# Kernel optimization log

Measured on AMD Instinct MI355X. Metric: run time of the kernel, lower is better.

The kernel has to match this reference:

```python
import jax, jax.numpy as jnp
import numpy as np

EPS = 1e-7   # keras.backend.epsilon() added before log in ctc_batch_cost
NEG = -1e30  # log-space 'zero'

B, T, C, L = 256, 1024, 96, 64


def setup_inputs() -> dict:
    key = jax.random.key(0)
    k1, k2 = jax.random.split(key)
    y_true = jax.random.randint(k1, (B, L), 0, C - 1, dtype=jnp.int32)  # labels in [0, C-2], blank = C-1
    y_pred = jax.random.uniform(k2, (B, T, C), dtype=jnp.float32)
    y_pred = y_pred / jnp.sum(y_pred, axis=-1, keepdims=True)  # valid softmax-like probabilities
    return {"y_true": y_true, "y_pred": y_pred}


def _ctc_loss(y_pred, y_true):
    # Faithful re-implementation of keras.backend.ctc_batch_cost with
    # input_length = T and label_length = L for every batch row.
    b, t, c = y_pred.shape
    l = y_true.shape[1]
    blank = c - 1
    s = 2 * l + 1  # extended label length (blanks interleaved)

    logp = jnp.log(y_pred + EPS)  # [B, T, C]

    # extended label sequence: blank, l0, blank, l1, ..., blank
    ext = jnp.full((b, s), blank, dtype=y_true.dtype).at[:, 1::2].set(y_true)  # [B, S]

    # emission log-probs per (t, b, s)
    lp = jnp.take_along_axis(logp, jnp.broadcast_to(ext[:, None, :], (b, t, s)), axis=2)  # [B, T, S]
    lp = jnp.transpose(lp, (1, 0, 2))  # [T, B, S]

    # skip transition s-2 -> s allowed iff ext[s] != blank and ext[s] != ext[s-2]
    ext_m2 = jnp.pad(ext, ((0, 0), (2, 0)), constant_values=-1)[:, :s]
    skip_ok = (ext != blank) & (ext != ext_m2)  # [B, S]

    alpha0 = jnp.full((b, s), NEG, dtype=logp.dtype)
    alpha0 = alpha0.at[:, 0].set(lp[0, :, 0]).at[:, 1].set(lp[0, :, 1])

    def step(alpha, lp_t):
        a1 = jnp.pad(alpha, ((0, 0), (1, 0)), constant_values=NEG)[:, :s]
        a2 = jnp.pad(alpha, ((0, 0), (2, 0)), constant_values=NEG)[:, :s]
        a2 = jnp.where(skip_ok, a2, NEG)
        new = jax.nn.logsumexp(jnp.stack([alpha, a1, a2]), axis=0) + lp_t
        return new, None

    alpha, _ = jax.lax.scan(step, alpha0, lp[1:])

    loss = -jax.nn.logsumexp(jnp.stack([alpha[:, s - 1], alpha[:, s - 2]]), axis=0)
    return loss[:, None]  # [B, 1], matching ctc_batch_cost


def reference(y_true, y_pred):
    return _ctc_loss(y_pred, y_true)
```

## Files before the change

kernel.cpp:

```cpp
#include <hip/hip_runtime.h>
#include <cstdint>


constexpr int BB = 256;
constexpr int TT = 1024;
constexpr int CC = 96;
constexpr int LL = 64;
constexpr int CT = 64;
constexpr int NCH = TT / CT;
constexpr int CHUNK_FLOATS = CT * CC;
constexpr int CHUNK_BYTES  = CHUNK_FLOATS*4;
#define EPSF 1e-7f

__device__ __forceinline__ float wf_shr1_f(float v) {
  int r = __builtin_amdgcn_update_dpp(0, __float_as_int(v), 0x138 , 0xF, 0xF, false);
  return __int_as_float(r);
}

template <int CTRL>
__device__ __forceinline__ float dpp_max(float v) {
  int r = __builtin_amdgcn_update_dpp(__float_as_int(v), __float_as_int(v), CTRL, 0xF, 0xF, false);
  return fmaxf(v, __int_as_float(r));
}

__device__ __forceinline__ void async16(void* lds, const void* g) {
  __builtin_amdgcn_global_load_lds((const __attribute__((address_space(1))) void*)g,
                                   (__attribute__((address_space(3))) void*)lds,
                                   16, 0, 0);
}

__global__ void __launch_bounds__(64, 1)
ctc_fwd(const int* __restrict__ y_true, const float* __restrict__ y_pred,
        float* __restrict__ out) {
  __shared__ alignas(16) float buf[2][CHUNK_FLOATS];
  const int b    = blockIdx.x;
  const int lane = threadIdx.x;

  const int lab  = y_true[b * LL + lane];
  const int labp = __builtin_amdgcn_update_dpp(-1, lab, 0x138, 0xF, 0xF, false);
  const float mskip = (lane > 0 && lab != labp) ? 1.0f : 0.0f;

  const char* src = (const char*)(y_pred + (size_t)b * (TT * CC));

  {
    const char* g0 = src + lane * 16;
#pragma unroll
    for (int j = 0; j < 24; ++j) async16((char*)&buf[0][0] + j * 1024, g0 + j * 1024);
    const char* g1 = src + CHUNK_BYTES + lane * 16;
#pragma unroll
    for (int j = 0; j < 24; ++j) async16((char*)&buf[1][0] + j * 1024, g1 + j * 1024);
  }

  float a0 = (lane == 0) ? 1.0f : 0.0f;
  float a1 = 0.0f;
  float a2 = 0.0f;
  int   scale = 0;

  for (int c = 0; c < NCH; ++c) {
    if (c < NCH - 1) asm volatile("s_waitcnt vmcnt(24)" ::: "memory");
    else             asm volatile("s_waitcnt vmcnt(0)"  ::: "memory");

    const float* bp = &buf[c & 1][0];
#pragma unroll
    for (int g8 = 0; g8 < 8; ++g8) {
#pragma unroll
      for (int u = 0; u < 8; ++u) {
        const int r = g8 * 8 + u;
        const float pl  = bp[r * CC + lab] + EPSF;
        const float pb  = bp[r * CC + (CC - 1)] + EPSF;
        const float a1p = wf_shr1_f(a1);
        const float na0 = (a0 + a1p) * pb;
        float s3 = a1 + a0;
        s3 = fmaf(a1p, mskip, s3);
        const float na1 = s3 * pl;
        const float na2 = (a2 + a1) * pb;
        a0 = na0; a1 = na1; a2 = na2;
      }
      float m = fmaxf(fmaxf(a0, a1), a2);
      m = dpp_max<0x111>(m);
      m = dpp_max<0x112>(m);
      m = dpp_max<0x114>(m);
      m = dpp_max<0x118>(m);
      m = dpp_max<0x142>(m);
      m = dpp_max<0x143>(m);
      const int mb = __builtin_amdgcn_readlane(__float_as_int(m), 63);
      const int k  = 227 - ((mb >> 23) & 0xFF);
      scale += k;
      a0 = ldexpf(a0, k);
      a1 = ldexpf(a1, k);
      a2 = ldexpf(a2, k);
    }

    if (c + 2 < NCH) {
      const char* g = src + (size_t)(c + 2) * CHUNK_BYTES + lane * 16;
      char* l = (char*)&buf[c & 1][0];
#pragma unroll
      for (int j = 0; j < 24; ++j) async16(l + j * 1024, g + j * 1024);
    }
  }

  if (lane == 63) {
    const float s = a1 + a2;
    out[b] = 0.693147180559945f * ((float)scale - log2f(s));
  }
}

extern "C" void kernel_launch(void* const* d_in, const int* in_sizes, int n_in,
                              void* d_out, int out_size, void* d_ws, size_t ws_size,
                              hipStream_t stream) {
  (void)in_sizes; (void)n_in; (void)d_ws; (void)ws_size; (void)out_size;
  const int*   y_true = (const int*)d_in[0];
  const float* y_pred = (const float*)d_in[1];
  float*       out    = (float*)d_out;
  ctc_fwd<<<BB, 64, 0, stream>>>(y_true, y_pred, out);
}
```

Before: 160.6 us.

## Replace LDS chunk staging with register-prefetched direct gathers of needed columns

Drops the 24KB-per-chunk async global-to-LDS copies of the full class dimension. Each lane now loads only the two probabilities it needs (its label and the blank) straight from global memory into a 4-slot register ring, prefetching 8-timestep groups three groups ahead. Rescaling now runs every 16 steps instead of every 8, with the exponent target lowered to leave headroom. This cuts the bytes moved and removes LDS traffic, at the cost of scattered 4-byte global loads whose latency must be hidden by the register pipeline.

```diff
diff --git a/kernel.cpp b/kernel.cpp
--- a/kernel.cpp
+++ b/kernel.cpp
@@ -6,10 +6,9 @@
 constexpr int TT = 1024;
 constexpr int CC = 96;
 constexpr int LL = 64;
-constexpr int CT = 64;
-constexpr int NCH = TT / CT;
-constexpr int CHUNK_FLOATS = CT * CC;
-constexpr int CHUNK_BYTES  = CHUNK_FLOATS*4;
+constexpr int G  = 8;
+constexpr int NG = TT / G;
+constexpr int SL = 4;
 #define EPSF 1e-7f
 
 __device__ __forceinline__ float wf_shr1_f(float v) {
@@ -23,16 +22,9 @@
   return fmaxf(v, __int_as_float(r));
 }
 
-__device__ __forceinline__ void async16(void* lds, const void* g) {
-  __builtin_amdgcn_global_load_lds((const __attribute__((address_space(1))) void*)g,
-                                   (__attribute__((address_space(3))) void*)lds,
-                                   16, 0, 0);
-}
-
 __global__ void __launch_bounds__(64, 1)
 ctc_fwd(const int* __restrict__ y_true, const float* __restrict__ y_pred,
         float* __restrict__ out) {
-  __shared__ alignas(16) float buf[2][CHUNK_FLOATS];
   const int b    = blockIdx.x;
   const int lane = threadIdx.x;
 
@@ -40,15 +32,18 @@
   const int labp = __builtin_amdgcn_update_dpp(-1, lab, 0x138, 0xF, 0xF, false);
   const float mskip = (lane > 0 && lab != labp) ? 1.0f : 0.0f;
 
-  const char* src = (const char*)(y_pred + (size_t)b * (TT * CC));
+  const float* __restrict__ p = y_pred + (size_t)b * (TT * CC);
 
-  {
-    const char* g0 = src + lane * 16;
+  float Pl[SL][G], Pb[SL][G];
+
 #pragma unroll
-    for (int j = 0; j < 24; ++j) async16((char*)&buf[0][0] + j * 1024, g0 + j * 1024);
-    const char* g1 = src + CHUNK_BYTES + lane * 16;
+  for (int g = 0; g < SL - 1; ++g) {
+    const float* q = p + g * (G * CC);
 #pragma unroll
-    for (int j = 0; j < 24; ++j) async16((char*)&buf[1][0] + j * 1024, g1 + j * 1024);
+    for (int u = 0; u < G; ++u) {
+      Pl[g][u] = q[u * CC + lab];
+      Pb[g][u] = q[u * CC + (CC - 1)];
+    }
   }
 
   float a0 = (lane == 0) ? 1.0f : 0.0f;
@@ -56,48 +51,59 @@
   float a2 = 0.0f;
   int   scale = 0;
 
-  for (int c = 0; c < NCH; ++c) {
-    if (c < NCH - 1) asm volatile("s_waitcnt vmcnt(24)" ::: "memory");
-    else             asm volatile("s_waitcnt vmcnt(0)"  ::: "memory");
+#define ISSUE(gidx, slot) do {                                         \
+    const float* q = p + (gidx) * (G * CC);                            \
+    _Pragma("unroll")                                                  \
+    for (int u = 0; u < G; ++u) {                                      \
+      Pl[slot][u] = q[u * CC + lab];                                   \
+      Pb[slot][u] = q[u * CC + (CC - 1)];                              \
+    }                                                                  \
+    __builtin_amdgcn_sched_barrier(0);                                 \
+  } while (0)
 
-    const float* bp = &buf[c & 1][0];
-#pragma unroll
-    for (int g8 = 0; g8 < 8; ++g8) {
-#pragma unroll
-      for (int u = 0; u < 8; ++u) {
-        const int r = g8 * 8 + u;
-        const float pl  = bp[r * CC + lab] + EPSF;
-        const float pb  = bp[r * CC + (CC - 1)] + EPSF;
-        const float a1p = wf_shr1_f(a1);
-        const float na0 = (a0 + a1p) * pb;
-        float s3 = a1 + a0;
-        s3 = fmaf(a1p, mskip, s3);
-        const float na1 = s3 * pl;
-        const float na2 = (a2 + a1) * pb;
-        a0 = na0; a1 = na1; a2 = na2;
-      }
-      float m = fmaxf(fmaxf(a0, a1), a2);
-      m = dpp_max<0x111>(m);
-      m = dpp_max<0x112>(m);
-      m = dpp_max<0x114>(m);
-      m = dpp_max<0x118>(m);
-      m = dpp_max<0x142>(m);
-      m = dpp_max<0x143>(m);
-      const int mb = __builtin_amdgcn_readlane(__float_as_int(m), 63);
-      const int k  = 227 - ((mb >> 23) & 0xFF);
-      scale += k;
-      a0 = ldexpf(a0, k);
-      a1 = ldexpf(a1, k);
-      a2 = ldexpf(a2, k);
-    }
+#define STEP8(slot) do {                                               \
+    _Pragma("unroll")                                                  \
+    for (int u = 0; u < G; ++u) {                                      \
+      const float PL  = Pl[slot][u] + EPSF;                            \
+      const float PB  = Pb[slot][u] + EPSF;                            \
+      const float a1p = wf_shr1_f(a1);                \
+      const float na0 = (a0 + a1p) * PB;              \
+      const float na2 = (a2 + a1) * PB;               \
+      const float na1 = fmaf(a1p, mskip, a1 + a0) * PL;      \
+      a0 = na0; a1 = na1; a2 = na2;                                    \
+    }                                                                  \
+  } while (0)
 
-    if (c + 2 < NCH) {
-      const char* g = src + (size_t)(c + 2) * CHUNK_BYTES + lane * 16;
-      char* l = (char*)&buf[c & 1][0];
-#pragma unroll
-      for (int j = 0; j < 24; ++j) async16(l + j * 1024, g + j * 1024);
-    }
+#define RESCALE do {                                                   \
+    float m = fmaxf(fmaxf(a0, a1), a2);                                \
+    m = dpp_max<0x111>(m);                             \
+    m = dpp_max<0x112>(m);                             \
+    m = dpp_max<0x114>(m);                             \
+    m = dpp_max<0x118>(m);                             \
+    m = dpp_max<0x142>(m);                           \
+    m = dpp_max<0x143>(m);     \
+    const int mb = __builtin_amdgcn_readlane(__float_as_int(m), 63);   \
+    const int k  = 223 - ((mb >> 23) & 0xFF);        \
+    scale += k;                                                        \
+    a0 = ldexpf(a0, k); a1 = ldexpf(a1, k); a2 = ldexpf(a2, k);        \
+  } while (0)
+
+#pragma unroll 1
+  for (int it = 0; it < NG / SL - 1; ++it) {
+    const int g0 = it * SL;
+    ISSUE(g0 + 3, 3); STEP8(0);
+    ISSUE(g0 + 4, 0); STEP8(1); RESCALE;
+    ISSUE(g0 + 5, 1); STEP8(2);
+    ISSUE(g0 + 6, 2); STEP8(3); RESCALE;
   }
+  ISSUE(127, 3); STEP8(0);
+  STEP8(1); RESCALE;
+  STEP8(2);
+  STEP8(3); RESCALE;
+
+#undef ISSUE
+#undef STEP8
+#undef RESCALE
 
   if (lane == 63) {
     const float s = a1 + a2;
```

New measurement: 179.7 us. +11.9%, slower.
